# Performance work log

Measured on AMD Instinct MI355X. Metric: run time of the kernel, lower is better.

The kernel has to match this reference:

```python
import jax, jax.numpy as jnp
import numpy as np

EMB_DIM = 512
R_DIM = 64
B, S = 8, 2048


def _lowrank_params(key):
    k1, k2, k3, k4 = jax.random.split(key, 4)
    s1 = 1.0 / np.sqrt(EMB_DIM)
    s2 = 1.0 / np.sqrt(R_DIM)
    w1 = jax.random.uniform(k1, (EMB_DIM, R_DIM), jnp.float32, -s1, s1)
    b1 = jax.random.uniform(k2, (R_DIM,), jnp.float32, -s1, s1)
    w2 = jax.random.uniform(k3, (R_DIM, EMB_DIM), jnp.float32, -s2, s2)
    b2 = jax.random.uniform(k4, (EMB_DIM,), jnp.float32, -s2, s2)
    return w1, b1, w2, b2


def setup_inputs() -> dict:
    key = jax.random.key(0)
    kx, km, kq, kk, kv = jax.random.split(key, 5)
    x = jax.random.normal(kx, (B, S, EMB_DIM), jnp.float32)
    attention_mask = jax.random.randint(km, (B, S), 0, 2, jnp.int32)
    q_w1, q_b1, q_w2, q_b2 = _lowrank_params(kq)
    k_w1, k_b1, k_w2, k_b2 = _lowrank_params(kk)
    v_w1, v_b1, v_w2, v_b2 = _lowrank_params(kv)
    return dict(x=x, attention_mask=attention_mask,
                q_w1=q_w1, q_b1=q_b1, q_w2=q_w2, q_b2=q_b2,
                k_w1=k_w1, k_b1=k_b1, k_w2=k_w2, k_b2=k_b2,
                v_w1=v_w1, v_b1=v_b1, v_w2=v_w2, v_b2=v_b2)


def _proj(x, w1, b1, w2, b2):
    # low-rank projection: emb -> r -> emb (two stacked Linears, no nonlinearity)
    return (x @ w1 + b1) @ w2 + b2


def reference(x, attention_mask,
              q_w1, q_b1, q_w2, q_b2,
              k_w1, k_b1, k_w2, k_b2,
              v_w1, v_b1, v_w2, v_b2):
    q = _proj(x, q_w1, q_b1, q_w2, q_b2)   # [B,S,E]
    k = _proj(x, k_w1, k_b1, k_w2, k_b2)   # [B,S,E]
    v = _proj(x, v_w1, v_b1, v_w2, v_b2)   # [B,S,E]
    scale = EMB_DIM ** (-0.5)
    scores = jnp.einsum('bse,bte->bst', q, k) * scale  # [B,S,S]
    m = attention_mask.astype(jnp.float32)
    scores = scores * m[:, :, None] * m[:, None, :]
    temp = jnp.einsum('bst,bte->bse', scores, v)       # [B,S,E]
    out = jax.nn.softmax(temp, axis=-1)                # softmax AFTER second bmm (non-standard)
    return out, q
```

## Files before the change

### kernel.cpp

```cpp
#include <hip/hip_runtime.h>
#include <hip/hip_bf16.h>

#define SCALE 0.044194173824159216f

typedef float f32x4 __attribute__((ext_vector_type(4)));
typedef __bf16 bf16x8 __attribute__((ext_vector_type(8)));

static __device__ __forceinline__ unsigned short f2bf(float f){
  unsigned u = __builtin_bit_cast(unsigned, f);
  u += 0x7fffu + ((u >> 16) & 1u);
  return (unsigned short)(u >> 16);
}

__global__ __launch_bounds__(256) void kB2(const float* __restrict__ x, const int* __restrict__ mask,
    const float* __restrict__ w1q, const float* __restrict__ b1q,
    const float* __restrict__ w1k, const float* __restrict__ b1k,
    const float* __restrict__ w1v, const float* __restrict__ b1v,
    const float* __restrict__ w2q, const float* __restrict__ b2q,
    const float* __restrict__ w2k, const float* __restrict__ b2k,
    unsigned short* __restrict__ Hq, float* __restrict__ part,
    float* __restrict__ Pm, unsigned short* __restrict__ W2qT){
  __shared__ __attribute__((aligned(16))) char smem[33792];
  unsigned short (*Ax)[40] = (unsigned short(*)[40])smem;
  unsigned short (*Bt)[40] = (unsigned short(*)[40])(smem + 5120);
  float (*ak)[66] = (float(*)[66])smem;
  float (*av)[66] = (float(*)[66])(smem + 16896);
  const int t = threadIdx.x, bid = blockIdx.x;
  const int lane = t & 63, wave = t >> 6;
  const int l15 = lane & 15, lg = lane >> 4, ks = lg * 8;
  const int r0 = bid * 64;
  f32x4 acc[12];
  #pragma unroll
  for (int j = 0; j < 12; j++) acc[j] = (f32x4){0.f,0.f,0.f,0.f};
  for (int k0 = 0; k0 < 512; k0 += 32){
    #pragma unroll
    for (int s = 0; s < 2; s++){
      int i = t + 256*s;
      int r = i >> 3, kq = (i & 7) * 4;
      float4 v = *(const float4*)(x + (size_t)(r0 + r)*512 + k0 + kq);
      ushort4 pk; pk.x = f2bf(v.x); pk.y = f2bf(v.y); pk.z = f2bf(v.z); pk.w = f2bf(v.w);
      *(ushort4*)&Ax[r][kq] = pk;
    }
    #pragma unroll
    for (int s = 0; s < 6; s++){
      int id = t + 256*s;
      int kk = id / 48, g = id - kk*48;
      int p = g >> 4, c4 = (g & 15) << 2;
      const float* w1p = (p==0)? w1q : ((p==1)? w1k : w1v);
      float4 v = *(const float4*)(w1p + (k0 + kk)*64 + c4);
      int n = (p << 6) | c4;
      Bt[n][kk]     = f2bf(v.x);
      Bt[n + 1][kk] = f2bf(v.y);
      Bt[n + 2][kk] = f2bf(v.z);
      Bt[n + 3][kk] = f2bf(v.w);
    }
    __syncthreads();
    const int arow = (wave << 4) | l15;
    bf16x8 af = *(const bf16x8*)&Ax[arow][ks];
    #pragma unroll
    for (int j = 0; j < 12; j++){
      bf16x8 bf = *(const bf16x8*)&Bt[j*16 + l15][ks];
      acc[j] = __builtin_amdgcn_mfma_f32_16x16x32_bf16(af, bf, acc[j], 0, 0, 0);
    }
    __syncthreads();
  }
  int rowl[4]; float mrow[4];
  #pragma unroll
  for (int rg = 0; rg < 4; rg++){
    rowl[rg] = (wave << 4) + (lg << 2) + rg;
    mrow[rg] = (float)mask[r0 + rowl[rg]];
  }
  #pragma unroll
  for (int j = 0; j < 4; j++){
    int c = (j << 4) | l15;
    float bias = b1q[c];
    #pragma unroll
    for (int rg = 0; rg < 4; rg++)
      Hq[(size_t)(r0 + rowl[rg])*64 + c] = f2bf(acc[j][rg] + bias);
  }
  #pragma unroll
  for (int j = 0; j < 4; j++){
    int c = (j << 4) | l15;
    float bias = b1k[c];
    #pragma unroll
    for (int rg = 0; rg < 4; rg++)
      ak[rowl[rg]][c] = (acc[4 + j][rg] + bias) * mrow[rg];
  }
  #pragma unroll
  for (int j = 0; j < 4; j++){
    int c = (j << 4) | l15;
    float bias = b1v[c];
    #pragma unroll
    for (int rg = 0; rg < 4; rg++)
      av[rowl[rg]][c] = acc[8 + j][rg] + bias;
  }
  if (t < 64){ ak[t][64] = (float)mask[r0 + t]; av[t][64] = 1.f; }
  __syncthreads();
  if (t < 169){
    int tj = t / 13, ti = t - tj*13;
    int i0 = ti * 5, j0 = tj * 5;
    float pacc[5][5];
    #pragma unroll
    for (int a = 0; a < 5; a++)
      #pragma unroll
      for (int v = 0; v < 5; v++) pacc[a][v] = 0.f;
    for (int r = 0; r < 64; r++){
      float a[5], v[5];
      #pragma unroll
      for (int ii = 0; ii < 5; ii++) a[ii] = ak[r][i0 + ii];
      #pragma unroll
      for (int jj = 0; jj < 5; jj++) v[jj] = av[r][j0 + jj];
      #pragma unroll
      for (int ii = 0; ii < 5; ii++)
        #pragma unroll
        for (int jj = 0; jj < 5; jj++) pacc[ii][jj] += a[ii] * v[jj];
    }
    float* pout = part + (size_t)bid * 4225;
    #pragma unroll
    for (int ii = 0; ii < 5; ii++)
      #pragma unroll
      for (int jj = 0; jj < 5; jj++)
        pout[(i0 + ii)*65 + (j0 + jj)] = pacc[ii][jj];
  }
  if (bid < 17){
    int id2 = bid*256 + t;
    if (id2 < 4225){
      int i = id2 / 65, j = id2 - i*65;
      const float* qi = (i < 64)? (w2q + i*512) : b2q;
      const float* kj = (j < 64)? (w2k + j*512) : b2k;
      float s = 0.f;
      for (int e = 0; e < 512; e += 4){
        float4 a = *(const float4*)(qi + e);
        float4 b = *(const float4*)(kj + e);
        s += a.x*b.x + a.y*b.y + a.z*b.z + a.w*b.w;
      }
      Pm[id2] = s * SCALE;
    }
  }
  if (bid >= 128){
    int id3 = (bid - 128)*256 + t;
    int e = id3 >> 6, r = id3 & 63;
    W2qT[id3] = f2bf(w2q[r*512 + e]);
  }
}

__global__ __launch_bounds__(256) void kR(const float* __restrict__ part, float* __restrict__ At){
  int g = blockIdx.x*256 + threadIdx.x;
  if (g < 33800){
    int b = g / 4225, e = g - b*4225;
    const float* p = part + (size_t)b*135200 + e;
    float s = 0.f;
    #pragma unroll
    for (int ch = 0; ch < 32; ch++) s += p[(size_t)ch*4225];
    At[g] = s;
  }
}

__global__ __launch_bounds__(256) void k3b(const float* __restrict__ At, const float* __restrict__ Pm,
    const float* __restrict__ w2v, const float* __restrict__ b2v,
    unsigned short* __restrict__ GtA, float* __restrict__ Gbias){
  __shared__ float Pl[65*66];
  __shared__ float Atl[65*66];
  __shared__ float T1l[65*66];
  const int t = threadIdx.x;
  const int b = blockIdx.x >> 3, ec = (blockIdx.x & 7) << 6;
  for (int id = t; id < 4225; id += 256){
    int i = id / 65, j = id - i*65;
    Pl[i*66 + j]  = Pm[id];
    Atl[i*66 + j] = At[(size_t)b*4225 + id];
  }
  __syncthreads();
  if (t < 169){
    int tj = t / 13, ti = t - tj*13;
    int i0 = ti * 5, j0 = tj * 5;
    float acc[5][5];
    #pragma unroll
    for (int a = 0; a < 5; a++)
      #pragma unroll
      for (int v = 0; v < 5; v++) acc[a][v] = 0.f;
    for (int k = 0; k < 65; k++){
      float a[5], vv[5];
      #pragma unroll
      for (int ii = 0; ii < 5; ii++) a[ii] = Pl[(i0 + ii)*66 + k];
      #pragma unroll
      for (int jj = 0; jj < 5; jj++) vv[jj] = Atl[k*66 + j0 + jj];
      #pragma unroll
      for (int ii = 0; ii < 5; ii++)
        #pragma unroll
        for (int jj = 0; jj < 5; jj++) acc[ii][jj] += a[ii] * vv[jj];
    }
    #pragma unroll
    for (int ii = 0; ii < 5; ii++)
      #pragma unroll
      for (int jj = 0; jj < 5; jj++) T1l[(i0 + ii)*66 + (j0 + jj)] = acc[ii][jj];
  }
  __syncthreads();
  for (int id = t; id < 4096; id += 256){
    int j = id >> 6, c = id & 63;
    Pl[j*66 + c] = w2v[j*512 + ec + c];
  }
  __syncthreads();
  if (t < 169){
    int tj = t / 13, ti = t - tj*13;
    int i0 = ti * 5, j0 = tj * 5;
    float acc[5][5];
    #pragma unroll
    for (int a = 0; a < 5; a++)
      #pragma unroll
      for (int v = 0; v < 5; v++) acc[a][v] = 0.f;
    for (int k = 0; k < 64; k++){
      float a[5], vv[5];
      #pragma unroll
      for (int ii = 0; ii < 5; ii++) a[ii] = T1l[(i0 + ii)*66 + k];
      #pragma unroll
      for (int jj = 0; jj < 5; jj++) vv[jj] = Pl[k*66 + j0 + jj];
      #pragma unroll
      for (int ii = 0; ii < 5; ii++)
        #pragma unroll
        for (int jj = 0; jj < 5; jj++) acc[ii][jj] += a[ii] * vv[jj];
    }
    #pragma unroll
    for (int ii = 0; ii < 5; ii++){
      int r = i0 + ii;
      float t64 = T1l[r*66 + 64];
      #pragma unroll
      for (int jj = 0; jj < 5; jj++){
        int ej = j0 + jj;
        if (ej < 64){
          int e = ec + ej;
          float s = acc[ii][jj] + t64 * b2v[e];
          if (r < 64) GtA[((size_t)b*512 + e)*64 + r] = f2bf(s);
          else        Gbias[b*512 + e] = s;
        }
      }
    }
  }
}

__global__ __launch_bounds__(256) void kD(const unsigned short* __restrict__ Hq, const unsigned short* __restrict__ W2qT,
    const unsigned short* __restrict__ GtA, const float* __restrict__ Gbias, const float* __restrict__ b2q,
    const int* __restrict__ mask, float* __restrict__ out, float* __restrict__ qout){
  const int t = threadIdx.x, lane = t & 63, wave = t >> 6;
  const int b = blockIdx.x >> 5, rc = (blockIdx.x & 31) << 6;
  const int l15 = lane & 15, lg = lane >> 4, ks = lg * 8;
  const size_t gr0 = (size_t)b*2048 + rc;
  const int arow = (wave << 4) | l15;
  const unsigned short* arp = Hq + (gr0 + arow)*64 + ks;
  bf16x8 a0 = *(const bf16x8*)arp;
  bf16x8 a1 = *(const bf16x8*)(arp + 32);
  const unsigned short* Bsrc = GtA + (size_t)b*512*64;
  f32x4 acc[32];
  #pragma unroll
  for (int f = 0; f < 32; f++) acc[f] = (f32x4){0.f,0.f,0.f,0.f};
  #pragma unroll
  for (int f = 0; f < 32; f++){
    int col = (f << 4) | l15;
    bf16x8 b0 = *(const bf16x8*)(Bsrc + col*64 + ks);
    bf16x8 b1 = *(const bf16x8*)(Bsrc + col*64 + 32 + ks);
    acc[f] = __builtin_amdgcn_mfma_f32_16x16x32_bf16(a0, b0, acc[f], 0, 0, 0);
    acc[f] = __builtin_amdgcn_mfma_f32_16x16x32_bf16(a1, b1, acc[f], 0, 0, 0);
  }
  #pragma unroll
  for (int f = 0; f < 32; f++){
    float gbv = Gbias[(b << 9) | (f << 4) | l15];
    #pragma unroll
    for (int rg = 0; rg < 4; rg++) acc[f][rg] += gbv;
  }
  #pragma unroll
  for (int rg = 0; rg < 4; rg++){
    int row = rc + (wave << 4) + (lg << 2) + rg;
    float m = (float)mask[b*2048 + row];
    float mx = -3.4e38f;
    #pragma unroll
    for (int f = 0; f < 32; f++){
      float v = acc[f][rg] * m;
      acc[f][rg] = v;
      mx = fmaxf(mx, v);
    }
    #pragma unroll
    for (int d = 1; d < 16; d <<= 1) mx = fmaxf(mx, __shfl_xor(mx, d, 64));
    float sum = 0.f;
    #pragma unroll
    for (int f = 0; f < 32; f++){
      float ev = __expf(acc[f][rg] - mx);
      acc[f][rg] = ev;
      sum += ev;
    }
    #pragma unroll
    for (int d = 1; d < 16; d <<= 1) sum += __shfl_xor(sum, d, 64);
    float inv = 1.f / sum;
    float* orow = out + ((size_t)b*2048 + row) * 512;
    #pragma unroll
    for (int f = 0; f < 32; f++) orow[(f << 4) | l15] = acc[f][rg] * inv;
  }
  #pragma unroll
  for (int f = 0; f < 32; f++) acc[f] = (f32x4){0.f,0.f,0.f,0.f};
  #pragma unroll
  for (int f = 0; f < 32; f++){
    int col = (f << 4) | l15;
    bf16x8 b0 = *(const bf16x8*)(W2qT + col*64 + ks);
    bf16x8 b1 = *(const bf16x8*)(W2qT + col*64 + 32 + ks);
    acc[f] = __builtin_amdgcn_mfma_f32_16x16x32_bf16(a0, b0, acc[f], 0, 0, 0);
    acc[f] = __builtin_amdgcn_mfma_f32_16x16x32_bf16(a1, b1, acc[f], 0, 0, 0);
  }
  #pragma unroll
  for (int f = 0; f < 32; f++){
    int col = (f << 4) | l15;
    float bias = b2q[col];
    #pragma unroll
    for (int rg = 0; rg < 4; rg++){
      int row = rc + (wave << 4) + (lg << 2) + rg;
      qout[((size_t)b*2048 + row) * 512 + col] = acc[f][rg] + bias;
    }
  }
}

extern "C" void kernel_launch(void* const* d_in, const int* in_sizes, int n_in,
                              void* d_out, int out_size, void* d_ws, size_t ws_size,
                              hipStream_t stream){
  const float* x    = (const float*)d_in[0];
  const int*   mask = (const int*)d_in[1];
  const float* q_w1 = (const float*)d_in[2];
  const float* q_b1 = (const float*)d_in[3];
  const float* q_w2 = (const float*)d_in[4];
  const float* q_b2 = (const float*)d_in[5];
  const float* k_w1 = (const float*)d_in[6];
  const float* k_b1 = (const float*)d_in[7];
  const float* k_w2 = (const float*)d_in[8];
  const float* k_b2 = (const float*)d_in[9];
  const float* v_w1 = (const float*)d_in[10];
  const float* v_b1 = (const float*)d_in[11];
  const float* v_w2 = (const float*)d_in[12];
  const float* v_b2 = (const float*)d_in[13];

  char* ws = (char*)d_ws;
  float*          Pm   = (float*)(ws + 0);
  unsigned short* W2qT = (unsigned short*)(ws + 32768);
  unsigned short* Hq   = (unsigned short*)(ws + 98304);
  float*          part = (float*)(ws + 2195456);
  float*          At   = (float*)(ws + 6521856);
  unsigned short* GtA  = (unsigned short*)(ws + 6657280);
  float*          Gbias= (float*)(ws + 7181568);

  float* out  = (float*)d_out;
  float* qout = out + (size_t)8*2048*512;

  kB2<<<256, 256, 0, stream>>>(x, mask, q_w1, q_b1, k_w1, k_b1, v_w1, v_b1,
                               q_w2, q_b2, k_w2, k_b2, Hq, part, Pm, W2qT);
  kR <<<133, 256, 0, stream>>>(part, At);
  k3b<<<64,  256, 0, stream>>>(At, Pm, v_w2, v_b2, GtA, Gbias);
  kD <<<256, 256, 0, stream>>>(Hq, W2qT, GtA, Gbias, q_b2, mask, out, qout);
}
```

Before: 107.5 us.

## Fuse partial-sum reduction into kCX and restage w1 loads with vectorized LDS writes

Removes the separate kR reduction kernel. Each kCX block now sums its batch's 32 partial 65x65 chunks directly into shared memory using vector loads, with the partial stride padded to 4228 so the loads stay aligned. The w1 staging in the first kernel is also rewritten so each lane reads four consecutive k rows and does a single 8-byte LDS store, instead of four scattered 2-byte stores. The cost is that the reduction now runs redundantly in the 8 blocks per batch and sits inside a 64-block kernel, trading one launch for more duplicated reads.

```diff
diff --git a/kernel.cpp b/kernel.cpp
--- a/kernel.cpp
+++ b/kernel.cpp
@@ -12,7 +12,7 @@
   return (unsigned short)(u >> 16);
 }
 
-__global__ __launch_bounds__(256) void kB2(const float* __restrict__ x, const int* __restrict__ mask,
+__global__ __launch_bounds__(256) void kB3(const float* __restrict__ x, const int* __restrict__ mask,
     const float* __restrict__ w1q, const float* __restrict__ b1q,
     const float* __restrict__ w1k, const float* __restrict__ b1k,
     const float* __restrict__ w1v, const float* __restrict__ b1v,
@@ -42,17 +42,17 @@
       *(ushort4*)&Ax[r][kq] = pk;
     }
     #pragma unroll
-    for (int s = 0; s < 6; s++){
-      int id = t + 256*s;
-      int kk = id / 48, g = id - kk*48;
-      int p = g >> 4, c4 = (g & 15) << 2;
+    for (int u = 0; u < 6; u++){
+      int uw = u*4 + wave;
+      int p = uw % 3, kq = uw / 3;
       const float* w1p = (p==0)? w1q : ((p==1)? w1k : w1v);
-      float4 v = *(const float4*)(w1p + (k0 + kk)*64 + c4);
-      int n = (p << 6) | c4;
-      Bt[n][kk]     = f2bf(v.x);
-      Bt[n + 1][kk] = f2bf(v.y);
-      Bt[n + 2][kk] = f2bf(v.z);
-      Bt[n + 3][kk] = f2bf(v.w);
+      const float* src = w1p + (size_t)(k0 + kq*4)*64 + lane;
+      ushort4 pk;
+      pk.x = f2bf(src[0]);
+      pk.y = f2bf(src[64]);
+      pk.z = f2bf(src[128]);
+      pk.w = f2bf(src[192]);
+      *(ushort4*)&Bt[p*64 + lane][kq*4] = pk;
     }
     __syncthreads();
     const int arow = (wave << 4) | l15;
@@ -115,7 +115,7 @@
         #pragma unroll
         for (int jj = 0; jj < 5; jj++) pacc[ii][jj] += a[ii] * v[jj];
     }
-    float* pout = part + (size_t)bid * 4225;
+    float* pout = part + (size_t)bid * 4228;
     #pragma unroll
     for (int ii = 0; ii < 5; ii++)
       #pragma unroll
@@ -144,30 +144,35 @@
   }
 }
 
-__global__ __launch_bounds__(256) void kR(const float* __restrict__ part, float* __restrict__ At){
-  int g = blockIdx.x*256 + threadIdx.x;
-  if (g < 33800){
-    int b = g / 4225, e = g - b*4225;
-    const float* p = part + (size_t)b*135200 + e;
-    float s = 0.f;
-    #pragma unroll
-    for (int ch = 0; ch < 32; ch++) s += p[(size_t)ch*4225];
-    At[g] = s;
-  }
-}
-
-__global__ __launch_bounds__(256) void k3b(const float* __restrict__ At, const float* __restrict__ Pm,
+__global__ __launch_bounds__(256) void kCX(const float* __restrict__ part, const float* __restrict__ Pm,
     const float* __restrict__ w2v, const float* __restrict__ b2v,
     unsigned short* __restrict__ GtA, float* __restrict__ Gbias){
   __shared__ float Pl[65*66];
-  __shared__ float Atl[65*66];
+  __shared__ float Atl[4228];
   __shared__ float T1l[65*66];
   const int t = threadIdx.x;
   const int b = blockIdx.x >> 3, ec = (blockIdx.x & 7) << 6;
   for (int id = t; id < 4225; id += 256){
     int i = id / 65, j = id - i*65;
-    Pl[i*66 + j]  = Pm[id];
-    Atl[i*66 + j] = At[(size_t)b*4225 + id];
+    Pl[i*66 + j] = Pm[id];
+  }
+  const float* pb = part + (size_t)b*32*4228;
+  for (int q = t; q < 1056; q += 256){
+    f32x4 s0 = (f32x4){0.f,0.f,0.f,0.f}, s1 = s0, s2 = s0, s3 = s0;
+    #pragma unroll
+    for (int ch = 0; ch < 32; ch += 4){
+      s0 += *(const f32x4*)(pb + (size_t)ch*4228     + q*4);
+      s1 += *(const f32x4*)(pb + (size_t)(ch+1)*4228 + q*4);
+      s2 += *(const f32x4*)(pb + (size_t)(ch+2)*4228 + q*4);
+      s3 += *(const f32x4*)(pb + (size_t)(ch+3)*4228 + q*4);
+    }
+    *(f32x4*)&Atl[q*4] = (s0 + s1) + (s2 + s3);
+  }
+  if (t == 0){
+    float s = 0.f;
+    #pragma unroll
+    for (int ch = 0; ch < 32; ch++) s += pb[(size_t)ch*4228 + 4224];
+    Atl[4224] = s;
   }
   __syncthreads();
   if (t < 169){
@@ -183,7 +188,7 @@
       #pragma unroll
       for (int ii = 0; ii < 5; ii++) a[ii] = Pl[(i0 + ii)*66 + k];
       #pragma unroll
-      for (int jj = 0; jj < 5; jj++) vv[jj] = Atl[k*66 + j0 + jj];
+      for (int jj = 0; jj < 5; jj++) vv[jj] = Atl[k*65 + j0 + jj];
       #pragma unroll
       for (int ii = 0; ii < 5; ii++)
         #pragma unroll
@@ -338,16 +343,14 @@
   unsigned short* W2qT = (unsigned short*)(ws + 32768);
   unsigned short* Hq   = (unsigned short*)(ws + 98304);
   float*          part = (float*)(ws + 2195456);
-  float*          At   = (float*)(ws + 6521856);
-  unsigned short* GtA  = (unsigned short*)(ws + 6657280);
-  float*          Gbias= (float*)(ws + 7181568);
+  unsigned short* GtA  = (unsigned short*)(ws + 6524928);
+  float*          Gbias= (float*)(ws + 7049216);
 
   float* out  = (float*)d_out;
   float* qout = out + (size_t)8*2048*512;
 
-  kB2<<<256, 256, 0, stream>>>(x, mask, q_w1, q_b1, k_w1, k_b1, v_w1, v_b1,
+  kB3<<<256, 256, 0, stream>>>(x, mask, q_w1, q_b1, k_w1, k_b1, v_w1, v_b1,
                                q_w2, q_b2, k_w2, k_b2, Hq, part, Pm, W2qT);
-  kR <<<133, 256, 0, stream>>>(part, At);
-  k3b<<<64,  256, 0, stream>>>(At, Pm, v_w2, v_b2, GtA, Gbias);
+  kCX<<<64,  256, 0, stream>>>(part, Pm, v_w2, v_b2, GtA, Gbias);
   kD <<<256, 256, 0, stream>>>(Hq, W2qT, GtA, Gbias, q_b2, mask, out, qout);
 }
```

Result: faster. 96.56 us (-10.1%).
